# Kernel tuning notes

Hardware: AMD Instinct MI355X
Metric: run time of the kernel (lower is better)

The kernel has to match this reference:

```python
import jax, jax.numpy as jnp
import numpy as np

K_CAND = 64
K_FINAL = 16
ALPHA = 0.5
CURV_RATIO = 0.5
EPS = 1e-8


def index_points(points, idx):
    # points: [B, N, C], idx: [B, ...] -> [B, ..., C]
    B, N, C = points.shape
    flat = idx.reshape(B, -1)
    g = jnp.take_along_axis(points, flat[..., None], axis=1)
    return g.reshape(idx.shape + (C,))


def fps(points, num_fps):
    # Furthest point sampling (matches pointnet2: starts from index 0).
    B, N, _ = points.shape
    barange = jnp.arange(B)

    def body(carry, _):
        mindist, last_idx = carry
        last_pt = points[barange, last_idx]                       # [B, 3]
        d = jnp.sum((points - last_pt[:, None, :]) ** 2, axis=-1)  # [B, N]
        mindist = jnp.minimum(mindist, d)
        next_idx = jnp.argmax(mindist, axis=1).astype(jnp.int32)
        return (mindist, next_idx), last_idx

    init = (jnp.full((B, N), 1e10, points.dtype), jnp.zeros((B,), jnp.int32))
    _, idxs = jax.lax.scan(body, init, None, length=num_fps)
    return idxs.T  # [B, num_fps]


def znorm(x):
    # per-cloud normalization over points dim, unbiased std like torch
    return (x - x.mean(axis=1, keepdims=True)) / (x.std(axis=1, ddof=1, keepdims=True) + EPS)


def reference(xyz, features, w1, b1, w2, b2, num_samples):
    B, N, _ = xyz.shape
    # --- candidate kNN via pairwise squared distances (same ordering as cdist) ---
    sq = jnp.sum(xyz * xyz, axis=-1)                               # [B, N]
    d2 = sq[:, :, None] + sq[:, None, :] - 2.0 * jnp.einsum('bnc,bmc->bnm', xyz, xyz)
    _, cand = jax.lax.top_k(-d2, K_CAND + 1)                       # smallest dists first
    cand = cand[:, :, 1:]                                          # drop self -> [B, N, 64]

    # --- learned neighbor scoring MLP on relative geometry/features ---
    nxyz = index_points(xyz, cand)                                 # [B, N, 64, 3]
    nfeat = index_points(features, cand)                           # [B, N, 64, C]
    rel_xyz = nxyz - xyz[:, :, None, :]
    rel_feat = nfeat - features[:, :, None, :]
    mlp_in = jnp.concatenate([rel_xyz, rel_feat], axis=-1)         # [B, N, 64, 3+C]
    h = jax.nn.gelu(mlp_in @ w1 + b1, approximate=False)
    scores = (h @ w2 + b2)[..., 0]                                 # [B, N, 64]
    _, top_in_cand = jax.lax.top_k(scores, K_FINAL)
    final_idx = jnp.take_along_axis(cand, top_in_cand, axis=2)     # [B, N, 16]

    # --- robust importance: curvature (3x3 SVD of cov) + feature variation ---
    n2xyz = index_points(xyz, final_idx)                           # [B, N, 16, 3]
    n2feat = index_points(features, final_idx)
    dxyz = n2xyz - xyz[:, :, None, :]
    cov = jnp.einsum('bnki,bnkj->bnij', dxyz, dxyz) / K_FINAL      # [B, N, 3, 3]
    s = jnp.linalg.svd(cov, compute_uv=False)                      # descending, [B, N, 3]
    l2, l1, l0 = s[..., 0] ** 2, s[..., 1] ** 2, s[..., 2] ** 2
    curvature = l0 / (l0 + l1 + l2 + EPS)
    dfeat = n2feat - features[:, :, None, :]
    feat_var = jnp.linalg.norm(dfeat, axis=-1).mean(axis=-1)       # [B, N]
    importance = znorm(curvature) + ALPHA * znorm(feat_var)

    # --- select curvature points, mask them, FPS for the rest ---
    num_curv = int(num_samples * CURV_RATIO)
    num_fps = num_samples - num_curv
    _, curv_idx = jax.lax.top_k(importance, num_curv)              # [B, num_curv]
    far_val = jnp.max(xyz) + 1.0
    barange = jnp.arange(B)[:, None]
    masked_xyz = xyz.at[barange, curv_idx].set(far_val)
    fps_idx = fps(masked_xyz, num_fps).astype(curv_idx.dtype)      # [B, num_fps]
    merged = jnp.concatenate([curv_idx, fps_idx], axis=1)          # [B, num_samples]
    sampled_xyz = index_points(xyz, merged)                        # [B, num_samples, 3]
    return sampled_xyz, merged


def setup_inputs() -> dict:
    key = jax.random.key(0)
    k1, k2, k3, k4 = jax.random.split(key, 4)
    B, N, C = 2, 8192, 64
    xyz = jax.random.normal(k1, (B, N, 3), jnp.float32)
    features = jax.random.normal(k2, (B, N, C), jnp.float32)
    fan_in1 = 3 + C
    w1 = jax.random.normal(k3, (fan_in1, 128), jnp.float32) / np.sqrt(fan_in1)
    b1 = jnp.zeros((128,), jnp.float32)
    w2 = jax.random.normal(k4, (128, 1), jnp.float32) / np.sqrt(128)
    b2 = jnp.zeros((1,), jnp.float32)
    return {"xyz": xyz, "features": features, "w1": w1, "b1": b1,
            "w2": w2, "b2": b2, "num_samples": 2048}
```

## Files before the change

kernel.cpp:

```cpp
#include <hip/hip_runtime.h>
#include <hip/hip_bf16.h>
#include <math.h>

#define N 8192
#define BATCH 2
#define NROWS (BATCH*N)

typedef float v2f __attribute__((ext_vector_type(2)));

static __device__ __forceinline__ float fsubr(float a, float b){ return __fadd_rn(a, -b); }
static __device__ __forceinline__ unsigned okey(float f){
  unsigned u = __float_as_uint(f);
  return (u & 0x80000000u) ? ~u : (u | 0x80000000u);
}

__global__ void aux_kernel(const float* __restrict__ xyz, float* __restrict__ xs, float* __restrict__ ys,
                           float* __restrict__ zs, float* __restrict__ sq, float4* __restrict__ mxyz,
                           unsigned* __restrict__ farkey){
  __shared__ unsigned lm[4];
  const int t = threadIdx.x;
  int i = blockIdx.x*256 + t;
  float m = -1e30f;
  if (i < NROWS){
    float x = xyz[i*3+0], y = xyz[i*3+1], z = xyz[i*3+2];
    xs[i]=x; ys[i]=y; zs[i]=z;
    sq[i] = __fadd_rn(__fadd_rn(__fmul_rn(x,x),__fmul_rn(y,y)),__fmul_rn(z,z));
    mxyz[i] = make_float4(x, y, z, 0.0f);
    m = fmaxf(fmaxf(x, y), z);
  }
  #pragma unroll
  for (int off = 32; off; off >>= 1) m = fmaxf(m, __shfl_down(m, off));
  if ((t & 63) == 0) lm[t >> 6] = okey(m);
  __syncthreads();
  if (t == 0){
    unsigned k = lm[0];
    k = k > lm[1] ? k : lm[1];
    k = k > lm[2] ? k : lm[2];
    k = k > lm[3] ? k : lm[3];
    atomicMax(farkey, k);
  }
}

__global__ __launch_bounds__(128) void q_kernel(const float* __restrict__ xyz, const float* __restrict__ feat,
                                                const float* __restrict__ w1, float* __restrict__ Q){
  __shared__ float sx[16][3];
  __shared__ float sf[16][64];
  const int t = threadIdx.x;
  const int row0 = blockIdx.x * 16;
  for (int j = t; j < 1024; j += 128) sf[j>>6][j&63] = feat[(size_t)row0*64 + j];
  if (t < 48) sx[t/3][t%3] = xyz[(size_t)row0*3 + t];
  __syncthreads();
  float acc[16];
  #pragma unroll
  for (int r = 0; r < 16; ++r) acc[r] = 0.0f;
  for (int c = 0; c < 3; ++c){
    float wv = w1[c*128 + t];
    #pragma unroll
    for (int r = 0; r < 16; ++r) acc[r] = fmaf(sx[r][c], wv, acc[r]);
  }
  for (int c = 0; c < 64; ++c){
    float wv = w1[(3+c)*128 + t];
    #pragma unroll
    for (int r = 0; r < 16; ++r) acc[r] = fmaf(sf[r][c], wv, acc[r]);
  }
  #pragma unroll
  for (int r = 0; r < 16; ++r) Q[(size_t)(row0+r)*128 + t] = acc[r];
}

#define BINBASE 0xBA00
__global__ __launch_bounds__(512) void knn_kernel(const float* __restrict__ xs, const float* __restrict__ ys,
                                                  const float* __restrict__ zs, const float* __restrict__ sq,
                                                  int* __restrict__ cand){
#pragma clang fp contract(off)
  __shared__ unsigned fk[N];
  __shared__ unsigned hist[2048];
  __shared__ unsigned long long win[1024];
  __shared__ int scal[8];
  const int t = threadIdx.x;
  const int base_row = blockIdx.x * 32;
  const int b = base_row >> 13;
  const int n0 = base_row & (N-1);
  const int pbase = b * N;
  v2f px[8], py[8], pz[8], ps[8];
  #pragma unroll
  for (int k = 0; k < 8; ++k){
    int i0 = t + (2*k)*512, i1 = t + (2*k+1)*512;
    px[k].x = xs[pbase+i0]; px[k].y = xs[pbase+i1];
    py[k].x = ys[pbase+i0]; py[k].y = ys[pbase+i1];
    pz[k].x = zs[pbase+i0]; pz[k].y = zs[pbase+i1];
    ps[k].x = sq[pbase+i0]; ps[k].y = sq[pbase+i1];
  }
  for (int r = 0; r < 32; ++r){
    const int n = n0 + r;
    const float qx = xs[pbase+n], qy = ys[pbase+n], qz = zs[pbase+n], qs = sq[pbase+n];
    #pragma unroll
    for (int j = 0; j < 4; ++j) hist[t + j*512] = 0;
    __syncthreads();
    #pragma unroll
    for (int k = 0; k < 8; ++k){
      v2f dot = px[k]*qx + py[k]*qy + pz[k]*qz;
      v2f dd  = (qs + ps[k]) - 2.0f*dot;
      unsigned u0 = okey(dd.x), u1 = okey(dd.y);
      fk[t + (2*k)*512] = u0;
      fk[t + (2*k+1)*512] = u1;
      int bin0 = (int)(u0 >> 16) - BINBASE; bin0 = bin0 < 0 ? 0 : (bin0 > 2047 ? 2047 : bin0);
      int bin1 = (int)(u1 >> 16) - BINBASE; bin1 = bin1 < 0 ? 0 : (bin1 > 2047 ? 2047 : bin1);
      atomicAdd(&hist[bin0], 1u);
      atomicAdd(&hist[bin1], 1u);
    }
    __syncthreads();
    if (t < 64){
      unsigned s = 0;
      for (int k2 = 0; k2 < 32; ++k2) s += hist[t*32 + ((k2 + t) & 31)];
      unsigned p = s;
      for (int off = 1; off < 64; off <<= 1){ unsigned v = (unsigned)__shfl_up((int)p, off); if (t >= off) p += v; }
      int excl = (int)(p - s);
      if (excl < 65 && (int)p >= 65){ scal[0] = t; scal[1] = excl; }
    }
    __syncthreads();
    {
      int g = scal[0];
      if (t < 32){
        unsigned s = hist[g*32 + t];
        unsigned p = s;
        for (int off = 1; off < 32; off <<= 1){ unsigned v = (unsigned)__shfl_up((int)p, off); if (t >= off) p += v; }
        int before = scal[1] + (int)(p - s);
        if (before < 65 && scal[1] + (int)p >= 65) scal[2] = g*32 + t;
      }
    }
    if (t == 0) scal[3] = 0;
    __syncthreads();
    int B1 = scal[2];
    unsigned limit = (B1 >= 2047) ? 0xFFFFFFFFu : ((unsigned)(BINBASE + B1 + 1) << 16);
    #pragma unroll
    for (int j = 0; j < 16; ++j){
      int i = t + j*512;
      unsigned u = fk[i];
      if (u < limit){
        int p = atomicAdd(&scal[3], 1);
        if (p < 1024) win[p] = ((unsigned long long)u << 32) | (unsigned)i;
      }
    }
    __syncthreads();
    int m = scal[3]; if (m > 1024) m = 1024;
    for (int e = t; e < m; e += 512){
      unsigned long long me = win[e];
      int rk = 0;
      for (int j2 = 0; j2 < m; ++j2) rk += (win[j2] < me) ? 1 : 0;
      if (rk >= 1 && rk < 65) cand[(size_t)(pbase + n)*64 + (rk-1)] = (int)(me & 0xFFFFFFFFull);
    }
    __syncthreads();
  }
}

__global__ __launch_bounds__(256) void score_kernel(const float* __restrict__ xyz, const float* __restrict__ feat,
                                                    const float* __restrict__ Q, const float* __restrict__ b1,
                                                    const float* __restrict__ w2, const float* __restrict__ b2,
                                                    const int* __restrict__ cand,
                                                    float* __restrict__ curv, float* __restrict__ fv){
  __shared__ float4 sb14[32], sw24[32];
  __shared__ int ssel[4][16];
  __shared__ float sdx[4][16], sdy[4][16], sdz[4][16], snrm[4][16];
  const int t = threadIdx.x;
  if (t < 32) sb14[t] = ((const float4*)b1)[t];
  else if (t < 64) sw24[t-32] = ((const float4*)w2)[t-32];
  __syncthreads();
  const int w = t >> 6, lane = t & 63;
  const int row = blockIdx.x*4 + w;
  const int b = row >> 13;
  const int pbase = b * N;
  const int n = row & (N-1);
  const int ck = cand[(size_t)row*64 + lane];
  const float4* Qn4 = (const float4*)(Q + (size_t)row * 128);
  const float4* Qc4 = (const float4*)(Q + (size_t)(pbase + ck) * 128);
  const float ks = 0.70710678118654752440f;
  float acc = 0.0f;
  for (int c = 0; c < 32; ++c){
    float4 qc = Qc4[c], qn = Qn4[c], bb = sb14[c], ww = sw24[c];
    float p0 = (qc.x - qn.x) + bb.x;
    float g0 = 0.5f * p0 * (1.0f + erff(p0 * ks));
    acc += g0 * ww.x;
    float p1 = (qc.y - qn.y) + bb.y;
    float g1 = 0.5f * p1 * (1.0f + erff(p1 * ks));
    acc += g1 * ww.y;
    float p2 = (qc.z - qn.z) + bb.z;
    float g2 = 0.5f * p2 * (1.0f + erff(p2 * ks));
    acc += g2 * ww.z;
    float p3 = (qc.w - qn.w) + bb.w;
    float g3 = 0.5f * p3 * (1.0f + erff(p3 * ks));
    acc += g3 * ww.w;
  }
  float score = acc + b2[0];
  unsigned key = okey(score);
  int rk = 0;
  for (int j = 0; j < 64; ++j){
    unsigned kj = (unsigned)__shfl((int)key, j);
    rk += (kj > key || (kj == key && j < lane)) ? 1 : 0;
  }
  float cx = xyz[(size_t)(pbase+ck)*3+0], cy = xyz[(size_t)(pbase+ck)*3+1], cz = xyz[(size_t)(pbase+ck)*3+2];
  float qxv = xyz[(size_t)(pbase+n)*3+0], qyv = xyz[(size_t)(pbase+n)*3+1], qzv = xyz[(size_t)(pbase+n)*3+2];
  if (rk < 16){
    ssel[w][rk] = ck;
    sdx[w][rk] = fsubr(cx, qxv);
    sdy[w][rk] = fsubr(cy, qyv);
    sdz[w][rk] = fsubr(cz, qzv);
  }
  __syncthreads();
  if (lane < 16){
    int si = ssel[w][lane];
    const float4* fc4 = (const float4*)(feat + (size_t)(pbase+si)*64);
    const float4* fn4 = (const float4*)(feat + (size_t)(pbase+n)*64);
    double s = 0.0;
    for (int c = 0; c < 16; ++c){
      float4 a = fc4[c], bq = fn4[c];
      float d0 = fsubr(a.x, bq.x); s += (double)d0 * (double)d0;
      float d1 = fsubr(a.y, bq.y); s += (double)d1 * (double)d1;
      float d2 = fsubr(a.z, bq.z); s += (double)d2 * (double)d2;
      float d3 = fsubr(a.w, bq.w); s += (double)d3 * (double)d3;
    }
    snrm[w][lane] = sqrtf((float)s);
  }
  __syncthreads();
  if (lane == 0){
    double cxx=0, cxy=0, cxz=0, cyy=0, cyz=0, czz=0;
    for (int k2 = 0; k2 < 16; ++k2){
      double dx = (double)sdx[w][k2], dy = (double)sdy[w][k2], dz = (double)sdz[w][k2];
      cxx += dx*dx; cxy += dx*dy; cxz += dx*dz; cyy += dy*dy; cyz += dy*dz; czz += dz*dz;
    }
    float fxx = (float)(cxx/16.0), fxy = (float)(cxy/16.0), fxz = (float)(cxz/16.0);
    float fyy = (float)(cyy/16.0), fyz = (float)(cyz/16.0), fzz = (float)(czz/16.0);
    double a = fxx, bbv = fyy, c = fzz, d = fxy, e = fyz, f = fxz;
    double p1 = d*d + f*f + e*e;
    double e0, e1, e2v;
    if (p1 == 0.0){ e0 = a; e1 = bbv; e2v = c; }
    else {
      double q = (a + bbv + c) / 3.0;
      double aa = a - q, bq = bbv - q, cc = c - q;
      double p2 = aa*aa + bq*bq + cc*cc + 2.0*p1;
      double p = sqrt(p2 / 6.0);
      double inv = 1.0 / p;
      double bxx = aa*inv, byy = bq*inv, bzz = cc*inv, bxy = d*inv, bxz = f*inv, byz = e*inv;
      double detB = bxx*(byy*bzz - byz*byz) - bxy*(bxy*bzz - byz*bxz) + bxz*(bxy*byz - byy*bxz);
      double rr = 0.5 * detB;
      rr = fmin(1.0, fmax(-1.0, rr));
      double phi = acos(rr) / 3.0;
      e0 = q + 2.0*p*cos(phi);
      e2v = q + 2.0*p*cos(phi + 2.0943951023931953);
      e1 = 3.0*q - e0 - e2v;
    }
    double s0 = fabs(e0), s1 = fabs(e1), s2d = fabs(e2v), tt;
    if (s0 < s1){ tt=s0; s0=s1; s1=tt; }
    if (s1 < s2d){ tt=s1; s1=s2d; s2d=tt; }
    if (s0 < s1){ tt=s0; s0=s1; s1=tt; }
    float sv0 = (float)s0, sv1 = (float)s1, sv2 = (float)s2d;
    float l2f = __fmul_rn(sv0,sv0), l1f = __fmul_rn(sv1,sv1), l0f = __fmul_rn(sv2,sv2);
    float den = __fadd_rn(__fadd_rn(__fadd_rn(l0f, l1f), l2f), 1e-8f);
    curv[row] = l0f / den;
    double fs = 0.0;
    for (int k2 = 0; k2 < 16; ++k2) fs += (double)snrm[w][k2];
    fv[row] = (float)(fs / 16.0);
  }
}

static __device__ __forceinline__ double blk_sum(double v, double* lds, int t){
  for (int off = 32; off; off >>= 1) v += __shfl_down(v, off);
  int w = t >> 6, lane = t & 63;
  if (lane == 0) lds[w] = v;
  __syncthreads();
  double r = (t < 16) ? lds[t] : 0.0;
  if (t < 64){ for (int off = 8; off; off >>= 1) r += __shfl_down(r, off); }
  if (t == 0) lds[0] = r;
  __syncthreads();
  double out = lds[0];
  __syncthreads();
  return out;
}

#define TBINBASE 0x3E00
__global__ __launch_bounds__(1024) void stats_topk_kernel(const float* __restrict__ curv, const float* __restrict__ fv,
                                                          int* __restrict__ merged, float4* __restrict__ mxyz,
                                                          const unsigned* __restrict__ farkey){
  __shared__ unsigned dk[N];
  __shared__ unsigned hist[2048];
  __shared__ unsigned long long win[2048];
  __shared__ int scal[8];
  __shared__ double lds[16];
  const int t = threadIdx.x;
  const int b = blockIdx.x;
  const int base = b * N;
  double sc = 0, sf = 0;
  for (int j = 0; j < 8; ++j){ int i = t + j*1024; sc += (double)curv[base+i]; sf += (double)fv[base+i]; }
  double Sc = blk_sum(sc, lds, t);
  double Sf = blk_sum(sf, lds, t);
  double mc = Sc/8192.0, mf = Sf/8192.0;
  double vc = 0, vf = 0;
  for (int j = 0; j < 8; ++j){ int i = t + j*1024;
    double d1 = (double)curv[base+i] - mc; vc += d1*d1;
    double d2 = (double)fv[base+i]  - mf; vf += d2*d2; }
  double Vc = blk_sum(vc, lds, t);
  double Vf = blk_sum(vf, lds, t);
  float mcf = (float)mc, mff = (float)mf;
  float dc = __fadd_rn((float)sqrt(Vc/8191.0), 1e-8f);
  float df = __fadd_rn((float)sqrt(Vf/8191.0), 1e-8f);
  #pragma unroll
  for (int j = 0; j < 2; ++j) hist[t + j*1024] = 0;
  if (t == 0) scal[3] = 0;
  __syncthreads();
  for (int j = 0; j < 8; ++j){
    int i = t + j*1024;
    float zc = fsubr(curv[base+i], mcf) / dc;
    float zf = fsubr(fv[base+i],  mff) / df;
    float impv = __fadd_rn(zc, __fmul_rn(0.5f, zf));
    unsigned u = ~okey(impv);
    dk[i] = u;
    int bin = (int)(u >> 16) - TBINBASE; bin = bin < 0 ? 0 : (bin > 2047 ? 2047 : bin);
    atomicAdd(&hist[bin], 1u);
  }
  __syncthreads();
  if (t < 64){
    unsigned s = 0;
    for (int k2 = 0; k2 < 32; ++k2) s += hist[t*32 + ((k2 + t) & 31)];
    unsigned p = s;
    for (int off = 1; off < 64; off <<= 1){ unsigned v = (unsigned)__shfl_up((int)p, off); if (t >= off) p += v; }
    int excl = (int)(p - s);
    if (excl < 1024 && (int)p >= 1024){ scal[0] = t; scal[1] = excl; }
  }
  __syncthreads();
  {
    int g = scal[0];
    if (t < 32){
      unsigned s = hist[g*32 + t];
      unsigned p = s;
      for (int off = 1; off < 32; off <<= 1){ unsigned v = (unsigned)__shfl_up((int)p, off); if (t >= off) p += v; }
      int before = scal[1] + (int)(p - s);
      if (before < 1024 && scal[1] + (int)p >= 1024) scal[2] = g*32 + t;
    }
  }
  __syncthreads();
  int B1 = scal[2];
  unsigned limit = (B1 >= 2047) ? 0xFFFFFFFFu : ((unsigned)(TBINBASE + B1 + 1) << 16);
  for (int j = 0; j < 8; ++j){
    int i = t + j*1024;
    unsigned u = dk[i];
    if (u < limit){
      int p = atomicAdd(&scal[3], 1);
      if (p < 2048) win[p] = ((unsigned long long)u << 13) | (unsigned)i;
    }
  }
  __syncthreads();
  int m = scal[3]; if (m > 2048) m = 2048;
  unsigned fk2 = *farkey;
  float rmax = (fk2 & 0x80000000u) ? __uint_as_float(fk2 & 0x7FFFFFFFu) : __uint_as_float(~fk2);
  const float far = __fadd_rn(rmax, 1.0f);
  for (int e = t; e < m; e += 1024){
    unsigned long long me = win[e];
    int rk = 0;
    for (int j2 = 0; j2 < m; ++j2) rk += (win[j2] < me) ? 1 : 0;
    if (rk < 1024){
      int idx = (int)(me & 0x1FFFull);
      merged[b*2048 + rk] = idx;
      mxyz[base + idx] = make_float4(far, far, far, 0.0f);
    }
  }
}

#define DPP_MAX64(CTRL) { \
    int nlo = __builtin_amdgcn_update_dpp(0, klo, (CTRL), 0xf, 0xf, true); \
    int nhi = __builtin_amdgcn_update_dpp(0, khi, (CTRL), 0xf, 0xf, true); \
    unsigned long long nk = ((unsigned long long)(unsigned)nhi << 32) | (unsigned)nlo; \
    unsigned long long ck = ((unsigned long long)(unsigned)khi << 32) | (unsigned)klo; \
    if (nk > ck){ klo = nlo; khi = nhi; } \
  }

__global__ __launch_bounds__(512, 2) void fps_kernel(const float4* __restrict__ mxyz, int* __restrict__ merged,
                                                     const float* __restrict__ xyz, float* __restrict__ out){
  extern __shared__ float4 stab[];
  __shared__ unsigned long long wkey[2][8];
  const int t = threadIdx.x;
  const int b = blockIdx.x;
  const int base = b * N;
  float px[16], py[16], pz[16], md[16];
  #pragma unroll
  for (int j = 0; j < 16; ++j){
    int i = t + j*512;
    float4 p = mxyz[base + i];
    px[j] = p.x; py[j] = p.y; pz[j] = p.z; md[j] = 1e10f;
    stab[i] = p;
  }
  if (t == 0) merged[b*2048 + 1024] = 0;
  __syncthreads();
  float4 w0 = stab[0];
  float lx = w0.x, ly = w0.y, lz = w0.z;
  for (int it = 0; it < 1023; ++it){
    float bestv = -1.0f; unsigned blow = 0u;
    #pragma unroll
    for (int j = 0; j < 16; ++j){
      float dx = fsubr(px[j], lx), dy = fsubr(py[j], ly), dz = fsubr(pz[j], lz);
      float d = __fadd_rn(__fadd_rn(__fmul_rn(dx,dx), __fmul_rn(dy,dy)), __fmul_rn(dz,dz));
      float nm = fminf(md[j], d);
      md[j] = nm;
      if (nm > bestv){ bestv = nm; blow = 8191u - (unsigned)(t + (j<<9)); }
    }
    unsigned long long key = ((unsigned long long)__float_as_uint(bestv) << 13) | (unsigned long long)blow;
    int klo = (int)(unsigned)(key & 0xFFFFFFFFull);
    int khi = (int)(unsigned)(key >> 32);
    DPP_MAX64(0x111)
    DPP_MAX64(0x112)
    DPP_MAX64(0x114)
    DPP_MAX64(0x118)
    DPP_MAX64(0x142)
    DPP_MAX64(0x143)
    if ((t & 63) == 63)
      wkey[it & 1][t >> 6] = ((unsigned long long)(unsigned)khi << 32) | (unsigned)klo;
    __syncthreads();
    const unsigned long long* wk = wkey[it & 1];
    unsigned long long k = wk[0];
    #pragma unroll
    for (int i2 = 1; i2 < 8; ++i2){ unsigned long long o = wk[i2]; if (o > k) k = o; }
    const int idx = 8191 - (int)(k & 0x1FFFull);
    if (t == 0) merged[b*2048 + 1024 + it + 1] = idx;
    float4 wv = stab[idx];
    lx = wv.x; ly = wv.y; lz = wv.z;
  }
  __threadfence_block();
  __syncthreads();
  for (int e = t; e < 2048; e += 512){
    int gi = b*2048 + e;
    int idx = merged[gi];
    out[12288 + gi] = (float)idx;
    const float* p = xyz + (size_t)(base + idx)*3;
    out[gi*3+0] = p[0]; out[gi*3+1] = p[1]; out[gi*3+2] = p[2];
  }
}

extern "C" void kernel_launch(void* const* d_in, const int* in_sizes, int n_in,
                              void* d_out, int out_size, void* d_ws, size_t ws_size,
                              hipStream_t stream){
  const float* xyz  = (const float*)d_in[0];
  const float* feat = (const float*)d_in[1];
  const float* w1   = (const float*)d_in[2];
  const float* b1   = (const float*)d_in[3];
  const float* w2   = (const float*)d_in[4];
  const float* b2   = (const float*)d_in[5];
  float* out = (float*)d_out;
  char* ws = (char*)d_ws;
  float*    Q      = (float*)   (ws);
  int*      cand   = (int*)     (ws + 8388608);
  float*    xs     = (float*)   (ws + 12582912);
  float*    ysv    = (float*)   (ws + 12648448);
  float*    zsv    = (float*)   (ws + 12713984);
  float*    sq     = (float*)   (ws + 12779520);
  float*    curv   = (float*)   (ws + 12845056);
  float*    fv     = (float*)   (ws + 12910592);
  int*      merged = (int*)     (ws + 13041664);
  unsigned* farkey = (unsigned*)(ws + 13058048);
  float4*   mxyz   = (float4*)  (ws + 13058112);

  hipMemsetAsync(farkey, 0, 4, stream);
  aux_kernel<<<64, 256, 0, stream>>>(xyz, xs, ysv, zsv, sq, mxyz, farkey);
  q_kernel<<<1024, 128, 0, stream>>>(xyz, feat, w1, Q);
  knn_kernel<<<512, 512, 0, stream>>>(xs, ysv, zsv, sq, cand);
  score_kernel<<<4096, 256, 0, stream>>>(xyz, feat, Q, b1, w2, b2, cand, curv, fv);
  stats_topk_kernel<<<2, 1024, 0, stream>>>(curv, fv, merged, mxyz, farkey);
  fps_kernel<<<2, 512, 131072, stream>>>(mxyz, merged, xyz, out);
}
```

Before: 1.605 ms.

## Replace kNN histogram radix selection with adaptive distance-threshold bisection

The kNN kernel no longer stores all 8192 keys in shared memory or builds a 2048-bin atomic histogram. Instead it keeps distances in registers and adjusts a distance threshold until between 65 and 1536 candidates fall below it. Counts come from DPP wavefront reductions, and the threshold is carried over from one row to the next. Freeing the shared memory allows two blocks per CU. The cost is extra block-wide sync iterations when the threshold misses, and a larger window to rank with the quadratic rank sort.

```diff
diff --git a/kernel.cpp b/kernel.cpp
--- a/kernel.cpp
+++ b/kernel.cpp
@@ -67,15 +67,15 @@
   for (int r = 0; r < 16; ++r) Q[(size_t)(row0+r)*128 + t] = acc[r];
 }
 
-#define BINBASE 0xBA00
-__global__ __launch_bounds__(512) void knn_kernel(const float* __restrict__ xs, const float* __restrict__ ys,
-                                                  const float* __restrict__ zs, const float* __restrict__ sq,
-                                                  int* __restrict__ cand){
+#define KNN_WIN 1536
+#define DPPSUMU(CTRL) { int o = __builtin_amdgcn_update_dpp(0, (int)c, (CTRL), 0xf, 0xf, true); c += (unsigned)o; }
+__global__ __launch_bounds__(512, 2) void knn_kernel(const float* __restrict__ xs, const float* __restrict__ ys,
+                                                     const float* __restrict__ zs, const float* __restrict__ sq,
+                                                     int* __restrict__ cand){
 #pragma clang fp contract(off)
-  __shared__ unsigned fk[N];
-  __shared__ unsigned hist[2048];
-  __shared__ unsigned long long win[1024];
-  __shared__ int scal[8];
+  __shared__ unsigned long long win[KNN_WIN];
+  __shared__ unsigned wcnt[2][8];
+  __shared__ int scal[2];
   const int t = threadIdx.x;
   const int base_row = blockIdx.x * 32;
   const int b = base_row >> 13;
@@ -90,59 +90,49 @@
     pz[k].x = zs[pbase+i0]; pz[k].y = zs[pbase+i1];
     ps[k].x = sq[pbase+i0]; ps[k].y = sq[pbase+i1];
   }
+  float T = 0.3f;
   for (int r = 0; r < 32; ++r){
     const int n = n0 + r;
     const float qx = xs[pbase+n], qy = ys[pbase+n], qz = zs[pbase+n], qs = sq[pbase+n];
-    #pragma unroll
-    for (int j = 0; j < 4; ++j) hist[t + j*512] = 0;
-    __syncthreads();
+    v2f d2[8];
     #pragma unroll
     for (int k = 0; k < 8; ++k){
       v2f dot = px[k]*qx + py[k]*qy + pz[k]*qz;
-      v2f dd  = (qs + ps[k]) - 2.0f*dot;
-      unsigned u0 = okey(dd.x), u1 = okey(dd.y);
-      fk[t + (2*k)*512] = u0;
-      fk[t + (2*k+1)*512] = u1;
-      int bin0 = (int)(u0 >> 16) - BINBASE; bin0 = bin0 < 0 ? 0 : (bin0 > 2047 ? 2047 : bin0);
-      int bin1 = (int)(u1 >> 16) - BINBASE; bin1 = bin1 < 0 ? 0 : (bin1 > 2047 ? 2047 : bin1);
-      atomicAdd(&hist[bin0], 1u);
-      atomicAdd(&hist[bin1], 1u);
+      d2[k]   = (qs + ps[k]) - 2.0f*dot;
+    }
+    float lo = 0.0f, hi = 0.0f;
+    bool hiset = false;
+    for (int itb = 0; itb < 32; ++itb){
+      unsigned c = 0;
+      #pragma unroll
+      for (int k = 0; k < 8; ++k){
+        c += (d2[k].x < T) ? 1u : 0u;
+        c += (d2[k].y < T) ? 1u : 0u;
+      }
+      DPPSUMU(0x111) DPPSUMU(0x112) DPPSUMU(0x114) DPPSUMU(0x118)
+      DPPSUMU(0x142) DPPSUMU(0x143)
+      if ((t & 63) == 63) wcnt[itb & 1][t >> 6] = c;
+      if (t == 0) scal[0] = 0;
+      __syncthreads();
+      const unsigned* wc = wcnt[itb & 1];
+      unsigned cnt = wc[0]+wc[1]+wc[2]+wc[3]+wc[4]+wc[5]+wc[6]+wc[7];
+      if (cnt >= 65u && cnt <= (unsigned)KNN_WIN) break;
+      if (cnt < 65u){ lo = T; T = hiset ? 0.5f*(lo+hi) : T*4.0f; }
+      else          { hi = T; hiset = true; T = 0.5f*(lo+hi); }
+    }
+    #pragma unroll
+    for (int k = 0; k < 8; ++k){
+      if (d2[k].x < T){
+        int p = atomicAdd(&scal[0], 1);
+        if (p < KNN_WIN) win[p] = ((unsigned long long)okey(d2[k].x) << 32) | (unsigned)(t + (2*k)*512);
+      }
+      if (d2[k].y < T){
+        int p = atomicAdd(&scal[0], 1);
+        if (p < KNN_WIN) win[p] = ((unsigned long long)okey(d2[k].y) << 32) | (unsigned)(t + (2*k+1)*512);
+      }
     }
     __syncthreads();
-    if (t < 64){
-      unsigned s = 0;
-      for (int k2 = 0; k2 < 32; ++k2) s += hist[t*32 + ((k2 + t) & 31)];
-      unsigned p = s;
-      for (int off = 1; off < 64; off <<= 1){ unsigned v = (unsigned)__shfl_up((int)p, off); if (t >= off) p += v; }
-      int excl = (int)(p - s);
-      if (excl < 65 && (int)p >= 65){ scal[0] = t; scal[1] = excl; }
-    }
-    __syncthreads();
-    {
-      int g = scal[0];
-      if (t < 32){
-        unsigned s = hist[g*32 + t];
-        unsigned p = s;
-        for (int off = 1; off < 32; off <<= 1){ unsigned v = (unsigned)__shfl_up((int)p, off); if (t >= off) p += v; }
-        int before = scal[1] + (int)(p - s);
-        if (before < 65 && scal[1] + (int)p >= 65) scal[2] = g*32 + t;
-      }
-    }
-    if (t == 0) scal[3] = 0;
-    __syncthreads();
-    int B1 = scal[2];
-    unsigned limit = (B1 >= 2047) ? 0xFFFFFFFFu : ((unsigned)(BINBASE + B1 + 1) << 16);
-    #pragma unroll
-    for (int j = 0; j < 16; ++j){
-      int i = t + j*512;
-      unsigned u = fk[i];
-      if (u < limit){
-        int p = atomicAdd(&scal[3], 1);
-        if (p < 1024) win[p] = ((unsigned long long)u << 32) | (unsigned)i;
-      }
-    }
-    __syncthreads();
-    int m = scal[3]; if (m > 1024) m = 1024;
+    int m = scal[0]; if (m > KNN_WIN) m = KNN_WIN;
     for (int e = t; e < m; e += 512){
       unsigned long long me = win[e];
       int rk = 0;
```

Result: slower. 4.266 ms (+165.7%).
